# Kernel tuning notes

Hardware: AMD Instinct MI355X
Metric: run time of the kernel (lower is better)

The kernel has to match this reference:

```python
import jax, jax.numpy as jnp
import numpy as np

N_HEAD = 16


def setup_inputs() -> dict:
    key = jax.random.key(0)
    ks = jax.random.split(key, 6)
    b, l, d = 4, 2048, 1024
    n_mem = 1000  # FAISS index is populated with 1000 random vectors per batch element
    return {
        "q": jax.random.normal(ks[0], (b, l, d), dtype=jnp.float32),
        "kv": jax.random.normal(ks[1], (b, l, d), dtype=jnp.float32),  # unused by forward (faithful)
        "mem_table": jax.random.uniform(ks[2], (b, n_mem, d), dtype=jnp.float32),
        "w_q": jax.random.normal(ks[3], (d, d), dtype=jnp.float32) / np.sqrt(d),
        "w_kv": jax.random.normal(ks[4], (d, 2 * (d // N_HEAD)), dtype=jnp.float32) / np.sqrt(d),
        "w_concat": jax.random.normal(ks[5], (d, d), dtype=jnp.float32) / np.sqrt(d),
        "topk": 1,
    }


def reference(q, kv, mem_table, w_q, w_kv, w_concat, topk):
    b, l, d = q.shape
    h = N_HEAD
    dh = d // h

    qp = q @ w_q  # (b, l, d)

    # Exact inner-product kNN (topk=1) replacing the per-batch FAISS HNSW search:
    # brute-force scores + argmax + gather of the nearest memory vector.
    knn_scores = jnp.einsum("bld,bnd->bln", qp, mem_table)  # (b, l, n_mem)
    idx = jnp.argmax(knn_scores, axis=-1)  # (b, l) int
    mem = jnp.take_along_axis(mem_table, idx[..., None], axis=1)  # (b, l, d)

    k, v = jnp.split(mem @ w_kv, 2, axis=-1)  # each (b, l, dh)

    qh = qp.reshape(b, l, h, dh).transpose(0, 2, 1, 3)  # (b, h, l, dh)
    # k, v are shared across heads (unsqueeze(1) in torch -> broadcast here)
    att = jnp.einsum("bhld,bmd->bhlm", qh, k) / np.float32(np.sqrt(dh))  # (b, h, l, l)
    att = jax.nn.softmax(att, axis=-1)
    out = jnp.einsum("bhlm,bmd->bhld", att, v)  # (b, h, l, dh)

    out = out.transpose(0, 2, 1, 3).reshape(b, l, d)
    return out @ w_concat
```

## Files before the change

### kernel.cpp

```cpp
#include <hip/hip_runtime.h>
#include <float.h>
#include <math.h>

#define BATCH 4
#define SEQ   2048
#define DIM   1024
#define NHEAD 16
#define DHEAD 64
#define NMEM  1000
#define NPAD  1024
#define ROWS  (BATCH*SEQ)

typedef __attribute__((ext_vector_type(8))) __bf16 bf16x8;
typedef __attribute__((ext_vector_type(4))) float  f32x4;

static __device__ inline f32x4 mfma16(bf16x8 a, bf16x8 b, f32x4 c) {
  return __builtin_amdgcn_mfma_f32_16x16x32_bf16(a, b, c, 0, 0, 0);
}

#define GLOAD16(g, l) __builtin_amdgcn_global_load_lds( \
    (const __attribute__((address_space(1))) unsigned int*)(g), \
    (__attribute__((address_space(3))) unsigned int*)(l), 16, 0, 0)

enum { MODE_C = 0, MODE_HILO = 1, MODE_ARGMAX = 2, MODE_KV = 3 };

template<int AF32, int NPROD, int MODE>
__global__ __launch_bounds__(256) void gemm3(
    const void* __restrict__ Ah_, const __bf16* __restrict__ Al,
    const __bf16* __restrict__ Bh, const __bf16* __restrict__ Bl,
    int rowsPerZ, long bStrideZ,
    float* __restrict__ C, __bf16* __restrict__ Oh, __bf16* __restrict__ Ol,
    float* __restrict__ pv, int* __restrict__ pi)
{
  extern __shared__ char smem[];
  __shared__ float s_pv[128];
  __shared__ int   s_pi[128];
  const int t = threadIdx.x;
  const int w = t >> 6, lane = t & 63, l15 = lane & 15, g = lane >> 4;
  const int wr = w >> 1, wc = w & 1;
  const int m0 = blockIdx.z * rowsPerZ + blockIdx.x * 128;
  const int n0 = blockIdx.y * 128;
  const __bf16* Bh_b = Bh + (size_t)blockIdx.z * bStrideZ;
  const __bf16* Bl_b = (NPROD == 3) ? (Bl + (size_t)blockIdx.z * bStrideZ) : (const __bf16*)0;

  char* sA  = smem;
  char* sAl = smem + 8192;
  char* sBh = smem + (AF32 ? 16384 : (NPROD == 3 ? 16384 : 8192));
  char* sBl = sBh + 8192;

  f32x4 acc[4][4];
  #pragma unroll
  for (int i = 0; i < 4; ++i)
    #pragma unroll
    for (int j = 0; j < 4; ++j) acc[i][j] = (f32x4){0.f, 0.f, 0.f, 0.f};

  for (int k0 = 0; k0 < DIM; k0 += 32) {
    if (AF32) {
      const float* Af = (const float*)Ah_;
      #pragma unroll
      for (int i = 0; i < 4; ++i) {
        int c = i * 256 + t;
        int r = c >> 3, s = c & 7;
        int sl = s ^ (r & 7);
        GLOAD16(&Af[(size_t)(m0 + r) * DIM + k0 + sl * 4], sA + i * 4096 + w * 1024);
      }
    } else {
      const __bf16* Ab = (const __bf16*)Ah_;
      #pragma unroll
      for (int i = 0; i < 2; ++i) {
        int c = i * 256 + t;
        int r = c >> 2, s = c & 3;
        int sl = s ^ (r & 3);
        GLOAD16(&Ab[(size_t)(m0 + r) * DIM + k0 + sl * 8], sA + i * 4096 + w * 1024);
        if (NPROD == 3)
          GLOAD16(&Al[(size_t)(m0 + r) * DIM + k0 + sl * 8], sAl + i * 4096 + w * 1024);
      }
    }
    #pragma unroll
    for (int i = 0; i < 2; ++i) {
      int c = i * 256 + t;
      int r = c >> 2, s = c & 3;
      int sl = s ^ (r & 3);
      GLOAD16(&Bh_b[(size_t)(n0 + r) * DIM + k0 + sl * 8], sBh + i * 4096 + w * 1024);
      if (NPROD == 3)
        GLOAD16(&Bl_b[(size_t)(n0 + r) * DIM + k0 + sl * 8], sBl + i * 4096 + w * 1024);
    }
    __syncthreads();

    bf16x8 ah[4], al[4], bh[4], bl[4];
    #pragma unroll
    for (int mi = 0; mi < 4; ++mi) {
      int r = wr * 64 + mi * 16 + l15;
      if (AF32) {
        int p0 = (2 * g) ^ (r & 7), p1 = (2 * g + 1) ^ (r & 7);
        float4 q0 = *(const float4*)(sA + r * 128 + p0 * 16);
        float4 q1 = *(const float4*)(sA + r * 128 + p1 * 16);
        float qq[8] = {q0.x, q0.y, q0.z, q0.w, q1.x, q1.y, q1.z, q1.w};
        #pragma unroll
        for (int j = 0; j < 8; ++j) {
          __bf16 h = (__bf16)qq[j];
          ah[mi][j] = h;
          al[mi][j] = (__bf16)(qq[j] - (float)h);
        }
      } else {
        int p = (g ^ (r & 3)) * 16;
        ah[mi] = *(const bf16x8*)(sA + r * 64 + p);
        if (NPROD == 3) al[mi] = *(const bf16x8*)(sAl + r * 64 + p);
      }
    }
    #pragma unroll
    for (int ni = 0; ni < 4; ++ni) {
      int r = wc * 64 + ni * 16 + l15;
      int p = (g ^ (r & 3)) * 16;
      bh[ni] = *(const bf16x8*)(sBh + r * 64 + p);
      if (NPROD == 3) bl[ni] = *(const bf16x8*)(sBl + r * 64 + p);
    }
    #pragma unroll
    for (int mi = 0; mi < 4; ++mi)
      #pragma unroll
      for (int ni = 0; ni < 4; ++ni) {
        acc[mi][ni] = mfma16(ah[mi], bh[ni], acc[mi][ni]);
        if (NPROD == 3) {
          acc[mi][ni] = mfma16(ah[mi], bl[ni], acc[mi][ni]);
          acc[mi][ni] = mfma16(al[mi], bh[ni], acc[mi][ni]);
        }
      }
    __syncthreads();
  }

  if (MODE == MODE_C) {
    #pragma unroll
    for (int mi = 0; mi < 4; ++mi)
      #pragma unroll
      for (int ni = 0; ni < 4; ++ni) {
        int col = n0 + wc * 64 + ni * 16 + l15;
        #pragma unroll
        for (int r = 0; r < 4; ++r) {
          int row = m0 + wr * 64 + mi * 16 + g * 4 + r;
          C[(size_t)row * DIM + col] = acc[mi][ni][r];
        }
      }
  } else if (MODE == MODE_HILO) {
    #pragma unroll
    for (int mi = 0; mi < 4; ++mi)
      #pragma unroll
      for (int ni = 0; ni < 4; ++ni) {
        int col = n0 + wc * 64 + ni * 16 + l15;
        #pragma unroll
        for (int r = 0; r < 4; ++r) {
          int row = m0 + wr * 64 + mi * 16 + g * 4 + r;
          float v = acc[mi][ni][r];
          __bf16 h = (__bf16)v;
          Oh[(size_t)row * DIM + col] = h;
          Ol[(size_t)row * DIM + col] = (__bf16)(v - (float)h);
        }
      }
  } else if (MODE == MODE_KV) {
    #pragma unroll
    for (int mi = 0; mi < 4; ++mi)
      #pragma unroll
      for (int ni = 0; ni < 4; ++ni) {
        int col = wc * 64 + ni * 16 + l15;
        #pragma unroll
        for (int r = 0; r < 4; ++r) {
          int gr = m0 + wr * 64 + mi * 16 + g * 4 + r;
          int bb = gr >> 10, n = gr & (NPAD - 1);
          __bf16 h = (__bf16)acc[mi][ni][r];
          if (col < DHEAD) Oh[(size_t)gr * DHEAD + col] = h;
          else             Ol[((size_t)bb * DHEAD + (col - DHEAD)) * NPAD + n] = h;
        }
      }
  } else {
    float vv[4][4]; int ii[4][4];
    #pragma unroll
    for (int mi = 0; mi < 4; ++mi)
      #pragma unroll
      for (int r = 0; r < 4; ++r) {
        float v = -FLT_MAX; int vi = 0x7fffffff;
        #pragma unroll
        for (int ni = 0; ni < 4; ++ni) {
          int col = n0 + wc * 64 + ni * 16 + l15;
          float s = (col < NMEM) ? acc[mi][ni][r] : -FLT_MAX;
          if (s > v) { v = s; vi = col; }
        }
        #pragma unroll
        for (int off = 1; off < 16; off <<= 1) {
          float ov = __shfl_xor(v, off);
          int   oi = __shfl_xor(vi, off);
          if (ov > v || (ov == v && oi < vi)) { v = ov; vi = oi; }
        }
        vv[mi][r] = v; ii[mi][r] = vi;
        if (wc == 0 && l15 == 0) {
          int lrow = wr * 64 + mi * 16 + g * 4 + r;
          s_pv[lrow] = v; s_pi[lrow] = vi;
        }
      }
    __syncthreads();
    if (wc == 1 && l15 == 0) {
      #pragma unroll
      for (int mi = 0; mi < 4; ++mi)
        #pragma unroll
        for (int r = 0; r < 4; ++r) {
          int lrow = wr * 64 + mi * 16 + g * 4 + r;
          float v0 = s_pv[lrow]; int i0 = s_pi[lrow];
          float v1 = vv[mi][r];  int i1 = ii[mi][r];
          float v; int vi;
          if (v1 > v0) { v = v1; vi = i1; } else { v = v0; vi = i0; }
          pv[(size_t)blockIdx.y * ROWS + m0 + lrow] = v;
          pi[(size_t)blockIdx.y * ROWS + m0 + lrow] = vi;
        }
    }
  }
}

__global__ __launch_bounds__(256) void knn_reduce(const float* __restrict__ pv,
                                                  const int* __restrict__ pi,
                                                  int* __restrict__ idx) {
  int r = blockIdx.x * 256 + threadIdx.x;
  float bv = -FLT_MAX; int bi = 0x7fffffff;
  #pragma unroll
  for (int c = 0; c < 8; ++c) {
    float v = pv[(size_t)c * ROWS + r];
    int   i = pi[(size_t)c * ROWS + r];
    if (v > bv || (v == bv && i < bi)) { bv = v; bi = i; }
  }
  idx[r] = bi;
}

__global__ __launch_bounds__(256) void hist_lc(const int* __restrict__ idx,
                                               float* __restrict__ lc) {
  __shared__ int hcnt[NPAD];
  const int t = threadIdx.x, b = blockIdx.x;
  #pragma unroll
  for (int i = 0; i < 4; ++i) hcnt[t + 256 * i] = 0;
  __syncthreads();
  #pragma unroll
  for (int i = 0; i < 8; ++i) atomicAdd(&hcnt[idx[b * SEQ + i * 256 + t]], 1);
  __syncthreads();
  #pragma unroll
  for (int i = 0; i < 4; ++i) {
    int n = t + 256 * i;
    int c = hcnt[n];
    lc[b * NPAD + n] = (n < NMEM && c > 0) ? logf((float)c) : -1e30f;
  }
}

__global__ __launch_bounds__(256) void attn_table(const __bf16* __restrict__ qph,
                                                  const __bf16* __restrict__ Ktab,
                                                  const __bf16* __restrict__ VtT,
                                                  const float* __restrict__ lc,
                                                  __bf16* __restrict__ attn_bf) {
  __shared__ char sK[8192];
  __shared__ char sV[8192];
  __shared__ __bf16 sP[4][32][72];
  const int t = threadIdx.x;
  const int wq = t >> 6, lane = t & 63, l15 = lane & 15, g = lane >> 4;
  const int b = blockIdx.z, h = blockIdx.y;
  const int q0 = blockIdx.x * 128 + wq * 32;

  bf16x8 qa[2][2];
  #pragma unroll
  for (int mi = 0; mi < 2; ++mi)
    #pragma unroll
    for (int ks = 0; ks < 2; ++ks)
      qa[mi][ks] = *(const bf16x8*)&qph[(size_t)(b * SEQ + q0 + mi * 16 + l15) * DIM +
                                        h * DHEAD + ks * 32 + g * 8];

  f32x4 O[2][4];
  #pragma unroll
  for (int mi = 0; mi < 2; ++mi)
    #pragma unroll
    for (int fd = 0; fd < 4; ++fd) O[mi][fd] = (f32x4){0.f, 0.f, 0.f, 0.f};
  float lsum[2][4];
  #pragma unroll
  for (int mi = 0; mi < 2; ++mi)
    #pragma unroll
    for (int r = 0; r < 4; ++r) lsum[mi][r] = 0.f;

  const __bf16* Kb = Ktab + (size_t)b * NPAD * DHEAD;
  const __bf16* Vb = VtT + (size_t)b * DHEAD * NPAD;
  const float* lcb = lc + b * NPAD;

  for (int n0 = 0; n0 < NPAD; n0 += 64) {
    #pragma unroll
    for (int i = 0; i < 2; ++i) {
      int c = i * 256 + t, row = c >> 3, s = c & 7, sl = s ^ (row & 7);
      GLOAD16(&Kb[(size_t)(n0 + row) * DHEAD + sl * 8], sK + i * 4096 + wq * 1024);
      GLOAD16(&Vb[(size_t)row * NPAD + n0 + sl * 8], sV + i * 4096 + wq * 1024);
    }
    __syncthreads();

    float lcv[4];
    #pragma unroll
    for (int ni = 0; ni < 4; ++ni) lcv[ni] = lcb[n0 + ni * 16 + l15];

    f32x4 S[2][4];
    #pragma unroll
    for (int mi = 0; mi < 2; ++mi)
      #pragma unroll
      for (int ni = 0; ni < 4; ++ni) S[mi][ni] = (f32x4){0.f, 0.f, 0.f, 0.f};
    #pragma unroll
    for (int ks = 0; ks < 2; ++ks) {
      bf16x8 kf[4];
      #pragma unroll
      for (int ni = 0; ni < 4; ++ni)
        kf[ni] = *(const bf16x8*)(sK + (ni * 16 + l15) * 128 +
                                  (((ks * 4 + g) ^ (l15 & 7)) * 16));
      #pragma unroll
      for (int mi = 0; mi < 2; ++mi)
        #pragma unroll
        for (int ni = 0; ni < 4; ++ni)
          S[mi][ni] = mfma16(qa[mi][ks], kf[ni], S[mi][ni]);
    }

    #pragma unroll
    for (int mi = 0; mi < 2; ++mi)
      #pragma unroll
      for (int r = 0; r < 4; ++r) {
        int row = mi * 16 + g * 4 + r;
        float rs = 0.f;
        #pragma unroll
        for (int ni = 0; ni < 4; ++ni) {
          float p = __expf(fmaf(S[mi][ni][r], 0.125f, lcv[ni]));
          rs += p;
          sP[wq][row][ni * 16 + l15] = (__bf16)p;
        }
        lsum[mi][r] += rs;
      }

    #pragma unroll
    for (int mi = 0; mi < 2; ++mi)
      #pragma unroll
      for (int ks = 0; ks < 2; ++ks) {
        bf16x8 pa = *(const bf16x8*)&sP[wq][mi * 16 + l15][ks * 32 + g * 8];
        #pragma unroll
        for (int fd = 0; fd < 4; ++fd) {
          bf16x8 vf = *(const bf16x8*)(sV + (fd * 16 + l15) * 128 +
                                       (((ks * 4 + g) ^ (l15 & 7)) * 16));
          O[mi][fd] = mfma16(pa, vf, O[mi][fd]);
        }
      }
    __syncthreads();
  }

  #pragma unroll
  for (int mi = 0; mi < 2; ++mi)
    #pragma unroll
    for (int r = 0; r < 4; ++r) {
      float rs = lsum[mi][r];
      #pragma unroll
      for (int off = 1; off < 16; off <<= 1) rs += __shfl_xor(rs, off);
      float inv = 1.f / rs;
      size_t row = (size_t)(b * SEQ + q0 + mi * 16 + g * 4 + r);
      #pragma unroll
      for (int fd = 0; fd < 4; ++fd)
        attn_bf[row * DIM + h * DHEAD + fd * 16 + l15] = (__bf16)(O[mi][fd][r] * inv);
    }
}

__global__ __launch_bounds__(256) void cast_w_t(const float* __restrict__ in,
                                                __bf16* __restrict__ oh,
                                                __bf16* __restrict__ ol,
                                                int writeLo) {
  __shared__ float tile[64][65];
  const int t = threadIdx.x;
  const int k0 = blockIdx.x * 64, n0 = blockIdx.y * 64;
  #pragma unroll
  for (int i = 0; i < 16; ++i) {
    int e = t + i * 256, r = e >> 6, c = e & 63;
    tile[r][c] = in[(size_t)(k0 + r) * DIM + n0 + c];
  }
  __syncthreads();
  #pragma unroll
  for (int i = 0; i < 16; ++i) {
    int e = t + i * 256, r = e >> 6, c = e & 63;
    float v = tile[c][r];
    __bf16 h = (__bf16)v;
    oh[(size_t)(n0 + r) * DIM + k0 + c] = h;
    if (writeLo) ol[(size_t)(n0 + r) * DIM + k0 + c] = (__bf16)(v - (float)h);
  }
}

__global__ __launch_bounds__(256) void cast_wkv_t(const float* __restrict__ in,
                                                  __bf16* __restrict__ oh,
                                                  __bf16* __restrict__ ol) {
  __shared__ float tile[64][65];
  const int t = threadIdx.x;
  const int k0 = blockIdx.x * 64, n0 = blockIdx.y * 64;
  #pragma unroll
  for (int i = 0; i < 16; ++i) {
    int e = t + i * 256, r = e >> 6, c = e & 63;
    tile[r][c] = in[(size_t)(k0 + r) * 128 + n0 + c];
  }
  __syncthreads();
  #pragma unroll
  for (int i = 0; i < 16; ++i) {
    int e = t + i * 256, r = e >> 6, c = e & 63;
    float v = tile[c][r];
    __bf16 h = (__bf16)v;
    oh[(size_t)(n0 + r) * DIM + k0 + c] = h;
    ol[(size_t)(n0 + r) * DIM + k0 + c] = (__bf16)(v - (float)h);
  }
}

__global__ __launch_bounds__(256) void cast_mem(const float* __restrict__ mem,
                                                __bf16* __restrict__ mh,
                                                __bf16* __restrict__ ml) {
  size_t e = ((size_t)blockIdx.x * 256 + threadIdx.x) * 8;
  int d = (int)(e & 1023);
  size_t rn = e >> 10;
  int n = (int)(rn & 1023), b = (int)(rn >> 10);
  bf16x8 h8, l8;
  if (n < NMEM) {
    const float* p = mem + ((size_t)b * NMEM + n) * DIM + d;
    #pragma unroll
    for (int j = 0; j < 8; ++j) {
      float v = p[j];
      __bf16 h = (__bf16)v;
      h8[j] = h; l8[j] = (__bf16)(v - (float)h);
    }
  } else {
    #pragma unroll
    for (int j = 0; j < 8; ++j) { h8[j] = (__bf16)0.f; l8[j] = (__bf16)0.f; }
  }
  *(bf16x8*)(mh + e) = h8;
  *(bf16x8*)(ml + e) = l8;
}

extern "C" void kernel_launch(void* const* d_in, const int* in_sizes, int n_in,
                              void* d_out, int out_size, void* d_ws, size_t ws_size,
                              hipStream_t stream) {
  const float* q        = (const float*)d_in[0];
  const float* mem      = (const float*)d_in[2];
  const float* w_q      = (const float*)d_in[3];
  const float* w_kv     = (const float*)d_in[4];
  const float* w_concat = (const float*)d_in[5];
  float* out = (float*)d_out;

  char* wsb = (char*)d_ws;
  __bf16* memh   = (__bf16*)(wsb + 0);
  __bf16* meml   = (__bf16*)(wsb + 8388608);
  __bf16* wqt_h  = (__bf16*)(wsb + 16777216);
  __bf16* wqt_l  = (__bf16*)(wsb + 18874368);
  __bf16* wct    = (__bf16*)(wsb + 20971520);
  __bf16* Ktab   = (__bf16*)(wsb + 23068672);
  __bf16* VtT    = (__bf16*)(wsb + 23592960);
  float*  lc     = (float*) (wsb + 24117248);
  float*  pv     = (float*) (wsb + 24133632);
  int*    pi     = (int*)   (wsb + 24395776);
  int*    idx    = (int*)   (wsb + 24657920);
  __bf16* wkvT_h = (__bf16*)(wsb + 24690688);
  __bf16* wkvT_l = (__bf16*)(wsb + 24952832);
  __bf16* qph    = (__bf16*)(wsb + 25214976);
  __bf16* qpl    = (__bf16*)(wsb + 41992192);
  __bf16* attn_bf = qpl;

  cast_w_t<<<dim3(16, 16), 256, 0, stream>>>(w_q, wqt_h, wqt_l, 1);
  cast_w_t<<<dim3(16, 16), 256, 0, stream>>>(w_concat, wct, (__bf16*)0, 0);
  cast_wkv_t<<<dim3(16, 2), 256, 0, stream>>>(w_kv, wkvT_h, wkvT_l);
  cast_mem<<<dim3(2048), 256, 0, stream>>>(mem, memh, meml);

  gemm3<1, 3, MODE_HILO><<<dim3(64, 8, 1), 256, 32768, stream>>>(
      (const void*)q, (const __bf16*)0, wqt_h, wqt_l, 0, 0,
      (float*)0, qph, qpl, (float*)0, (int*)0);

  gemm3<0, 3, MODE_KV><<<dim3(BATCH * NPAD / 128, 1, 1), 256, 32768, stream>>>(
      (const void*)memh, meml, wkvT_h, wkvT_l, 0, 0,
      (float*)0, Ktab, VtT, (float*)0, (int*)0);

  gemm3<0, 3, MODE_ARGMAX><<<dim3(16, 8, 4), 256, 32768, stream>>>(
      (const void*)qph, qpl, memh, meml, 2048, (long)NPAD * DIM,
      (float*)0, (__bf16*)0, (__bf16*)0, pv, pi);
  knn_reduce<<<dim3(32), 256, 0, stream>>>(pv, pi, idx);

  hist_lc<<<dim3(BATCH), 256, 0, stream>>>(idx, lc);

  attn_table<<<dim3(SEQ / 128, NHEAD, BATCH), 256, 0, stream>>>(qph, Ktab, VtT, lc, attn_bf);

  gemm3<0, 1, MODE_C><<<dim3(64, 8, 1), 256, 16384, stream>>>(
      (const void*)attn_bf, (const __bf16*)0, wct, (const __bf16*)0, 0, 0,
      out, (__bf16*)0, (__bf16*)0, (float*)0, (int*)0);
}
```

Baseline: 273.3 us.

## Read K/V tiles directly from global in attention, fold softmax scale into exp2

The attention-table kernel no longer stages K and V tiles through shared memory with block-wide barriers. Each wave now loads its MFMA fragments straight from global memory, relying on the cache since the table is small and shared. The softmax scale and log2(e) are folded into the query projection output, and the histogram log-counts use log2, so the inner loop uses a bare exp2. The V table columns are permuted at write time so each lane can store its P values as one packed vector, at the cost of duplicated global/cache traffic across waves.

```diff
diff --git a/kernel.cpp b/kernel.cpp
--- a/kernel.cpp
+++ b/kernel.cpp
@@ -10,8 +10,10 @@
 #define NMEM  1000
 #define NPAD  1024
 #define ROWS  (BATCH*SEQ)
+#define QSCALE 0.18033688011112042f
 
 typedef __attribute__((ext_vector_type(8))) __bf16 bf16x8;
+typedef __attribute__((ext_vector_type(4))) __bf16 bf16x4;
 typedef __attribute__((ext_vector_type(4))) float  f32x4;
 
 static __device__ inline f32x4 mfma16(bf16x8 a, bf16x8 b, f32x4 c) {
@@ -149,7 +151,7 @@
         #pragma unroll
         for (int r = 0; r < 4; ++r) {
           int row = m0 + wr * 64 + mi * 16 + g * 4 + r;
-          float v = acc[mi][ni][r];
+          float v = acc[mi][ni][r] * QSCALE;
           __bf16 h = (__bf16)v;
           Oh[(size_t)row * DIM + col] = h;
           Ol[(size_t)row * DIM + col] = (__bf16)(v - (float)h);
@@ -166,8 +168,12 @@
           int gr = m0 + wr * 64 + mi * 16 + g * 4 + r;
           int bb = gr >> 10, n = gr & (NPAD - 1);
           __bf16 h = (__bf16)acc[mi][ni][r];
-          if (col < DHEAD) Oh[(size_t)gr * DHEAD + col] = h;
-          else             Ol[((size_t)bb * DHEAD + (col - DHEAD)) * NPAD + n] = h;
+          if (col < DHEAD) {
+            Oh[(size_t)gr * DHEAD + col] = h;
+          } else {
+            int np = (n & ~63) | ((n & 15) << 2) | ((n >> 4) & 3);
+            Ol[((size_t)bb * DHEAD + (col - DHEAD)) * NPAD + np] = h;
+          }
         }
       }
   } else {
@@ -241,17 +247,15 @@
   for (int i = 0; i < 4; ++i) {
     int n = t + 256 * i;
     int c = hcnt[n];
-    lc[b * NPAD + n] = (n < NMEM && c > 0) ? logf((float)c) : -1e30f;
+    lc[b * NPAD + n] = (n < NMEM && c > 0) ? log2f((float)c) : -1e30f;
   }
 }
 
 __global__ __launch_bounds__(256) void attn_table(const __bf16* __restrict__ qph,
                                                   const __bf16* __restrict__ Ktab,
-                                                  const __bf16* __restrict__ VtT,
-                                                  const float* __restrict__ lc,
+                                                  const __bf16* __restrict__ VtTp,
+                                                  const float* __restrict__ lc2,
                                                   __bf16* __restrict__ attn_bf) {
-  __shared__ char sK[8192];
-  __shared__ char sV[8192];
   __shared__ __bf16 sP[4][32][72];
   const int t = threadIdx.x;
   const int wq = t >> 6, lane = t & 63, l15 = lane & 15, g = lane >> 4;
@@ -278,18 +282,10 @@
     for (int r = 0; r < 4; ++r) lsum[mi][r] = 0.f;
 
   const __bf16* Kb = Ktab + (size_t)b * NPAD * DHEAD;
-  const __bf16* Vb = VtT + (size_t)b * DHEAD * NPAD;
-  const float* lcb = lc + b * NPAD;
+  const __bf16* Vb = VtTp + (size_t)b * DHEAD * NPAD;
+  const float* lcb = lc2 + b * NPAD;
 
   for (int n0 = 0; n0 < NPAD; n0 += 64) {
-    #pragma unroll
-    for (int i = 0; i < 2; ++i) {
-      int c = i * 256 + t, row = c >> 3, s = c & 7, sl = s ^ (row & 7);
-      GLOAD16(&Kb[(size_t)(n0 + row) * DHEAD + sl * 8], sK + i * 4096 + wq * 1024);
-      GLOAD16(&Vb[(size_t)row * NPAD + n0 + sl * 8], sV + i * 4096 + wq * 1024);
-    }
-    __syncthreads();
-
     float lcv[4];
     #pragma unroll
     for (int ni = 0; ni < 4; ++ni) lcv[ni] = lcb[n0 + ni * 16 + l15];
@@ -304,8 +300,7 @@
       bf16x8 kf[4];
       #pragma unroll
       for (int ni = 0; ni < 4; ++ni)
-        kf[ni] = *(const bf16x8*)(sK + (ni * 16 + l15) * 128 +
-                                  (((ks * 4 + g) ^ (l15 & 7)) * 16));
+        kf[ni] = *(const bf16x8*)&Kb[(size_t)(n0 + ni * 16 + l15) * DHEAD + ks * 32 + g * 8];
       #pragma unroll
       for (int mi = 0; mi < 2; ++mi)
         #pragma unroll
@@ -318,29 +313,32 @@
       #pragma unroll
       for (int r = 0; r < 4; ++r) {
         int row = mi * 16 + g * 4 + r;
+        bf16x4 p4;
         float rs = 0.f;
         #pragma unroll
         for (int ni = 0; ni < 4; ++ni) {
-          float p = __expf(fmaf(S[mi][ni][r], 0.125f, lcv[ni]));
+          float p = __builtin_amdgcn_exp2f(S[mi][ni][r] + lcv[ni]);
           rs += p;
-          sP[wq][row][ni * 16 + l15] = (__bf16)p;
-        }
+          p4[ni] = (__bf16)p;
+        }
+        *(bf16x4*)&sP[wq][row][l15 * 4] = p4;
         lsum[mi][r] += rs;
       }
 
     #pragma unroll
-    for (int mi = 0; mi < 2; ++mi)
-      #pragma unroll
-      for (int ks = 0; ks < 2; ++ks) {
+    for (int ks = 0; ks < 2; ++ks) {
+      bf16x8 vf[4];
+      #pragma unroll
+      for (int fd = 0; fd < 4; ++fd)
+        vf[fd] = *(const bf16x8*)&Vb[(size_t)(fd * 16 + l15) * NPAD + n0 + ks * 32 + g * 8];
+      #pragma unroll
+      for (int mi = 0; mi < 2; ++mi) {
         bf16x8 pa = *(const bf16x8*)&sP[wq][mi * 16 + l15][ks * 32 + g * 8];
         #pragma unroll
-        for (int fd = 0; fd < 4; ++fd) {
-          bf16x8 vf = *(const bf16x8*)(sV + (fd * 16 + l15) * 128 +
-                                       (((ks * 4 + g) ^ (l15 & 7)) * 16));
-          O[mi][fd] = mfma16(pa, vf, O[mi][fd]);
-        }
-      }
-    __syncthreads();
+        for (int fd = 0; fd < 4; ++fd)
+          O[mi][fd] = mfma16(pa, vf[fd], O[mi][fd]);
+      }
+    }
   }
 
   #pragma unroll
```

Result: slower. 350.6 us (+28.3%).
